# Kernel optimization log

Measured on AMD Instinct MI355X. Metric: run time of the kernel, lower is better.

Reference implementation:

```python
import jax, jax.numpy as jnp
import numpy as np

DIM = 512
BATCH, SEQ = 4, 4096


def setup_inputs() -> dict:
    key = jax.random.key(0)
    kx, kq, kk, kv, ko = jax.random.split(key, 5)
    s = DIM ** -0.5  # fan-in style init scale for stability
    return {
        "x": jax.random.normal(kx, (BATCH, SEQ, DIM), dtype=jnp.float32),
        "Wq": jax.random.normal(kq, (DIM, DIM), dtype=jnp.float32) * s,
        "Wk": jax.random.normal(kk, (DIM, DIM), dtype=jnp.float32) * s,
        "Wv": jax.random.normal(kv, (DIM, DIM), dtype=jnp.float32) * s,
        "Wo": jax.random.normal(ko, (DIM, DIM), dtype=jnp.float32) * s,
    }


def reference(x, Wq, Wk, Wv, Wo):
    # x: [B, S, D]; projections (torch Linear, no bias -> x @ W here)
    q = jnp.einsum('bsd,dk->bsk', x, Wq)  # [B,S,K]
    k = jnp.einsum('bsd,dk->bsk', x, Wk)  # [B,S,K]
    v = jnp.einsum('bsd,dv->bsv', x, Wv)  # [B,S,V]

    # sequential recurrence: M_t = M_{t-1} + v_t k_t^T ; y_t = M_t q_t
    def step(M, qkv_t):
        q_t, k_t, v_t = qkv_t  # each [B, K] / [B, V]
        M = M + v_t[:, :, None] * k_t[:, None, :]  # [B, V, K]
        y_t = jnp.einsum('bvk,bk->bv', M, q_t)
        return M, y_t

    M0 = jnp.zeros((x.shape[0], Wv.shape[1], Wk.shape[1]), dtype=x.dtype)
    qT = jnp.swapaxes(q, 0, 1)  # [S,B,K]
    kT = jnp.swapaxes(k, 0, 1)
    vT = jnp.swapaxes(v, 0, 1)
    _, ys = jax.lax.scan(step, M0, (qT, kT, vT))  # ys: [S,B,V]
    y = jnp.swapaxes(ys, 0, 1)  # [B,S,V]
    return jnp.einsum('bsv,vd->bsd', y, Wo)
```

## Files before the change

### kernel.cpp

```cpp
#include <hip/hip_runtime.h>
#include <hip/hip_bf16.h>

typedef __attribute__((ext_vector_type(8))) short bf16x8;
typedef __attribute__((ext_vector_type(4))) float f32x4;

__device__ inline short f2bf(float f) {
    __hip_bfloat16 h = __float2bfloat16(f);
    short s;
    __builtin_memcpy(&s, &h, 2);
    return s;
}
__device__ inline float bf2f(short s) {
    unsigned int u = ((unsigned int)(unsigned short)s) << 16;
    float f;
    __builtin_memcpy(&f, &u, 4);
    return f;
}

__device__ inline void cp16_async(const void* g, void* l) {
    __builtin_amdgcn_global_load_lds(
        (const __attribute__((address_space(1))) void*)g,
        (__attribute__((address_space(3))) void*)l, 16, 0, 0);
}


__global__ void cast_x_kernel(const float* __restrict__ x, short* __restrict__ out, int n4) {
    int i = blockIdx.x * 256 + threadIdx.x;
    if (i < n4) {
        float4 f = ((const float4*)x)[i];
        union { short s[4]; int2 v; } u;
        u.s[0] = f2bf(f.x); u.s[1] = f2bf(f.y); u.s[2] = f2bf(f.z); u.s[3] = f2bf(f.w);
        ((int2*)out)[i] = u.v;
    }
}

__global__ void transpose_cast_w4(const float* __restrict__ W0, const float* __restrict__ W1,
                                  const float* __restrict__ W2, const float* __restrict__ W3,
                                  short* __restrict__ W4T) {
    int i = blockIdx.x * 256 + threadIdx.x;
    int w = i >> 18;
    int r = i & 262143;
    int n = r >> 9, k = r & 511;
    const float* W = (w == 0) ? W0 : (w == 1) ? W1 : (w == 2) ? W2 : W3;
    W4T[i] = f2bf(W[k * 512 + n]);
}

__global__ void transpose_bf16(const short* __restrict__ in, short* __restrict__ out) {
    __shared__ short sT[64][72];
    const int t0 = blockIdx.x * 64, f0 = blockIdx.y * 64, b = blockIdx.z;
    const short* ip = in + (size_t)b * 4096 * 512;
    short* op = out + (size_t)b * 512 * 4096;
#pragma unroll
    for (int p = 0; p < 2; ++p) {
        int lin = p * 256 + threadIdx.x;
        int row = lin >> 3, col8 = (lin & 7) * 8;
        short tmp[8];
        *(int4*)tmp = *(const int4*)&ip[(size_t)(t0 + row) * 512 + f0 + col8];
#pragma unroll
        for (int s = 0; s < 8; ++s) sT[col8 + s][row] = tmp[s];
    }
    __syncthreads();
#pragma unroll
    for (int p = 0; p < 2; ++p) {
        int lin = p * 256 + threadIdx.x;
        int fr = lin >> 3, tc8 = (lin & 7) * 8;
        int4 v = *(const int4*)&sT[fr][tc8];
        *(int4*)&op[(size_t)(f0 + fr) * 4096 + t0 + tc8] = v;
    }
}


#define LDS_DECL __shared__ short sA0[4096], sA1[4096], sB0[4096], sB1[4096]

__device__ inline void mfma_kloop64(const short* __restrict__ A, int lda,
                                    const short* __restrict__ B, int ldb,
                                    int Kd, f32x4* acc,
                                    short* sA0, short* sA1, short* sB0, short* sB1) {
    const int tid = threadIdx.x, lane = tid & 63, wv = tid >> 6;
    const int quad = lane >> 4, lr = lane & 15;
    const int wr = (wv >> 1) * 64, wc = (wv & 1) * 64;
    const int c0 = tid, c1 = tid + 256;
    const int r0 = c0 >> 2, k80 = (c0 & 3) * 8;
    const int r1 = c1 >> 2, k81 = (c1 & 3) * 8;

    for (int k0 = 0; k0 < Kd; k0 += 64) {
        __syncthreads();
        cp16_async(A + (size_t)r0 * lda + k0 + k80,      sA0 + c0 * 8);
        cp16_async(A + (size_t)r1 * lda + k0 + k81,      sA0 + c1 * 8);
        cp16_async(A + (size_t)r0 * lda + k0 + 32 + k80, sA1 + c0 * 8);
        cp16_async(A + (size_t)r1 * lda + k0 + 32 + k81, sA1 + c1 * 8);
        cp16_async(B + (size_t)r0 * ldb + k0 + k80,      sB0 + c0 * 8);
        cp16_async(B + (size_t)r1 * ldb + k0 + k81,      sB0 + c1 * 8);
        cp16_async(B + (size_t)r0 * ldb + k0 + 32 + k80, sB1 + c0 * 8);
        cp16_async(B + (size_t)r1 * ldb + k0 + 32 + k81, sB1 + c1 * 8);
        __syncthreads();
#pragma unroll
        for (int half = 0; half < 2; ++half) {
            const short* pa = half ? sA1 : sA0;
            const short* pb = half ? sB1 : sB0;
            bf16x8 af[4], bfr[4];
#pragma unroll
            for (int i = 0; i < 4; ++i)
                af[i] = *(const bf16x8*)&pa[(wr + i * 16 + lr) * 32 + quad * 8];
#pragma unroll
            for (int j = 0; j < 4; ++j)
                bfr[j] = *(const bf16x8*)&pb[(wc + j * 16 + lr) * 32 + quad * 8];
#pragma unroll
            for (int i = 0; i < 4; ++i)
#pragma unroll
                for (int j = 0; j < 4; ++j)
                    acc[i * 4 + j] = __builtin_amdgcn_mfma_f32_16x16x32_bf16(af[i], bfr[j], acc[i * 4 + j], 0, 0, 0);
        }
    }
}

__device__ inline void store_out(float* p, float v) { *p = v; }
__device__ inline void store_out(short* p, float v) { *p = f2bf(v); }

template <typename OutT>
__device__ inline void store_tile128(OutT* C, int ldc, const f32x4* acc) {
    const int lane = threadIdx.x & 63, wv = threadIdx.x >> 6;
    const int quad = lane >> 4, lr = lane & 15;
    const int wr = (wv >> 1) * 64, wc = (wv & 1) * 64;
#pragma unroll
    for (int i = 0; i < 4; ++i)
#pragma unroll
        for (int j = 0; j < 4; ++j)
#pragma unroll
            for (int r = 0; r < 4; ++r)
                store_out(&C[(size_t)(wr + i * 16 + quad * 4 + r) * ldc + wc + j * 16 + lr],
                          acc[i * 4 + j][r]);
}


__global__ __launch_bounds__(256, 2) void gemm_qk(const short* __restrict__ Xb,
                                                  const short* __restrict__ WqkT,
                                                  short* __restrict__ Qb, short* __restrict__ Kb) {
    LDS_DECL;
    const short* At = Xb + (size_t)blockIdx.x * 128 * 512;
    const short* Bt = WqkT + (size_t)blockIdx.y * 128 * 512;
    short* Cbase = (blockIdx.y < 4) ? Qb : Kb;
    int n0 = (blockIdx.y & 3) * 128;
    short* Ct = Cbase + (size_t)blockIdx.x * 128 * 512 + n0;
    f32x4 acc[16];
#pragma unroll
    for (int i = 0; i < 16; ++i) acc[i] = (f32x4){0.f, 0.f, 0.f, 0.f};
    mfma_kloop64(At, 512, Bt, 512, 512, acc, sA0, sA1, sB0, sB1);
    store_tile128(Ct, 512, acc);
}

__global__ __launch_bounds__(256, 2) void gemm_vt(const short* __restrict__ WvT,
                                                  const short* __restrict__ Xb,
                                                  short* __restrict__ Vt) {
    LDS_DECL;
    const int b = blockIdx.z;
    const short* At = WvT + (size_t)blockIdx.x * 128 * 512;
    const short* Bt = Xb + ((size_t)b * 4096 + blockIdx.y * 128) * 512;
    short* Ct = Vt + (size_t)b * 512 * 4096 + (size_t)blockIdx.x * 128 * 4096 + blockIdx.y * 128;
    f32x4 acc[16];
#pragma unroll
    for (int i = 0; i < 16; ++i) acc[i] = (f32x4){0.f, 0.f, 0.f, 0.f};
    mfma_kloop64(At, 512, Bt, 512, 512, acc, sA0, sA1, sB0, sB1);
    store_tile128(Ct, 4096, acc);
}

template <typename OutT>
__global__ __launch_bounds__(256, 2) void gemm128(const short* __restrict__ A, int lda,
                                                  const short* __restrict__ B, int ldb,
                                                  OutT* __restrict__ C, int ldc, int Kd) {
    LDS_DECL;
    const short* At = A + (size_t)blockIdx.x * 128 * lda;
    const short* Bt = B + (size_t)blockIdx.y * 128 * ldb;
    OutT* Ct = C + (size_t)blockIdx.x * 128 * ldc + blockIdx.y * 128;
    f32x4 acc[16];
#pragma unroll
    for (int i = 0; i < 16; ++i) acc[i] = (f32x4){0.f, 0.f, 0.f, 0.f};
    mfma_kloop64(At, lda, Bt, ldb, Kd, acc, sA0, sA1, sB0, sB1);
    store_tile128(Ct, ldc, acc);
}


__global__ __launch_bounds__(256, 2) void phaseA(const short* __restrict__ Vt,
                                                 const short* __restrict__ Kt,
                                                 short* __restrict__ AM) {
    LDS_DECL;
    const int bc = blockIdx.z, b = bc >> 4, c = bc & 15;
    const short* Ap = Vt + ((size_t)b * 512 + blockIdx.x * 128) * 4096 + c * 256;
    const short* Bp = Kt + ((size_t)b * 512 + blockIdx.y * 128) * 4096 + c * 256;
    short* Cp = AM + (size_t)bc * 262144 + (size_t)blockIdx.x * 128 * 512 + blockIdx.y * 128;
    f32x4 acc[16];
#pragma unroll
    for (int i = 0; i < 16; ++i) acc[i] = (f32x4){0.f, 0.f, 0.f, 0.f};
    mfma_kloop64(Ap, 4096, Bp, 4096, 256, acc, sA0, sA1, sB0, sB1);
    store_tile128(Cp, 512, acc);
}

__global__ void scan_kernel(short* __restrict__ AM) {
    int i = blockIdx.x * 256 + threadIdx.x;
    int b = i >> 15;
    int vk8 = i & 32767;
    size_t base = (size_t)b * 16 * 262144 + (size_t)vk8 * 8;
    float acc[8];
#pragma unroll
    for (int s = 0; s < 8; ++s) acc[s] = 0.f;
    for (int c = 0; c < 16; ++c) {
        short* p = AM + base + (size_t)c * 262144;
        short in8[8];
        *(int4*)in8 = *(const int4*)p;
        short out8[8];
#pragma unroll
        for (int s = 0; s < 8; ++s) out8[s] = f2bf(acc[s]);
        *(int4*)p = *(const int4*)out8;
#pragma unroll
        for (int s = 0; s < 8; ++s) acc[s] += bf2f(in8[s]);
    }
}

__global__ __launch_bounds__(256, 2) void phaseS(const short* __restrict__ Q,
                                                 const short* __restrict__ K,
                                                 short* __restrict__ P) {
    LDS_DECL;
    const int bc = blockIdx.z, b = bc >> 4, c = bc & 15;
    const int mt = blockIdx.x, nt = blockIdx.y;
    if (mt < nt) return;
    short* Pt = P + (size_t)bc * 65536 + (size_t)mt * 128 * 256 + nt * 128;
    const short* Ap = Q + ((size_t)(b * 4096 + c * 256 + mt * 128)) * 512;
    const short* Bp = K + ((size_t)(b * 4096 + c * 256 + nt * 128)) * 512;
    f32x4 acc[16];
#pragma unroll
    for (int i = 0; i < 16; ++i) acc[i] = (f32x4){0.f, 0.f, 0.f, 0.f};
    mfma_kloop64(Ap, 512, Bp, 512, 512, acc, sA0, sA1, sB0, sB1);
    const int lane = threadIdx.x & 63, wv = threadIdx.x >> 6;
    const int quad = lane >> 4, lr = lane & 15;
    const int wr = (wv >> 1) * 64, wc = (wv & 1) * 64;
    const bool diag = (mt == nt);
#pragma unroll
    for (int i = 0; i < 4; ++i)
#pragma unroll
        for (int j = 0; j < 4; ++j)
#pragma unroll
            for (int r = 0; r < 4; ++r) {
                int t = wr + i * 16 + quad * 4 + r;
                int jj = wc + j * 16 + lr;
                float v = (!diag || jj <= t) ? acc[i * 4 + j][r] : 0.f;
                Pt[(size_t)t * 256 + jj] = f2bf(v);
            }
}

__global__ __launch_bounds__(256, 2) void phaseY(const short* __restrict__ Q,
                                                 const short* __restrict__ Mpre,
                                                 const short* __restrict__ P,
                                                 const short* __restrict__ Vt,
                                                 short* __restrict__ Y) {
    LDS_DECL;
    const int bc = blockIdx.z, b = bc >> 4, c = bc & 15;
    const int mt = blockIdx.x, nt = blockIdx.y;
    f32x4 acc[16];
#pragma unroll
    for (int i = 0; i < 16; ++i) acc[i] = (f32x4){0.f, 0.f, 0.f, 0.f};
    const short* Ai = Q + ((size_t)(b * 4096 + c * 256 + mt * 128)) * 512;
    const short* Bi = Mpre + (size_t)bc * 262144 + (size_t)nt * 128 * 512;
    mfma_kloop64(Ai, 512, Bi, 512, 512, acc, sA0, sA1, sB0, sB1);
    const short* Ap = P + (size_t)bc * 65536 + (size_t)mt * 128 * 256;
    const short* Bv = Vt + ((size_t)b * 512 + nt * 128) * 4096 + c * 256;
    mfma_kloop64(Ap, 256, Bv, 4096, (mt + 1) * 128, acc, sA0, sA1, sB0, sB1);
    short* Cp = Y + ((size_t)(b * 4096 + c * 256 + mt * 128)) * 512 + nt * 128;
    store_tile128(Cp, 512, acc);
}


extern "C" void kernel_launch(void* const* d_in, const int* in_sizes, int n_in,
                              void* d_out, int out_size, void* d_ws, size_t ws_size,
                              hipStream_t stream) {
    const float* x  = (const float*)d_in[0];
    const float* Wq = (const float*)d_in[1];
    const float* Wk = (const float*)d_in[2];
    const float* Wv = (const float*)d_in[3];
    const float* Wo = (const float*)d_in[4];
    float* out = (float*)d_out;

    const size_t NTD = 16384 * 512;

    short* ws  = (short*)d_ws;
    short* Xb  = ws;
    short* Qb  = Xb + NTD;
    short* Kb  = Qb + NTD;
    short* Kt  = Kb + NTD;
    short* Vt  = Kt + NTD;
    short* P   = Vt + NTD;
    short* W4T = P + 4194304;
    short* AM  = W4T + 1048576;
    short* Yb  = Kb;

    short* WqT = W4T;
    short* WvT = W4T + 2 * 262144;
    short* WoT = W4T + 3 * 262144;

    cast_x_kernel<<<8192, 256, 0, stream>>>(x, Xb, (int)(NTD / 4));
    transpose_cast_w4<<<4096, 256, 0, stream>>>(Wq, Wk, Wv, Wo, W4T);

    gemm_qk<<<dim3(128, 8), 256, 0, stream>>>(Xb, WqT, Qb, Kb);
    gemm_vt<<<dim3(4, 32, 4), 256, 0, stream>>>(WvT, Xb, Vt);
    transpose_bf16<<<dim3(64, 8, 4), 256, 0, stream>>>(Kb, Kt);

    phaseA<<<dim3(4, 4, 64), 256, 0, stream>>>(Vt, Kt, AM);
    scan_kernel<<<512, 256, 0, stream>>>(AM);
    phaseS<<<dim3(2, 2, 64), 256, 0, stream>>>(Qb, Kb, P);
    phaseY<<<dim3(2, 4, 64), 256, 0, stream>>>(Qb, AM, P, Vt, Yb);

    gemm128<float><<<dim3(128, 4), 256, 0, stream>>>(Yb, 512, WoT, 512, out, 512, 512);
}
```

Before: 231.5 us.

## Merge independent launches and compute K transpose via extra GEMM instead of transpose kernel

Merges the x cast and weight transpose-cast into one prep kernel, and merges the Q/K, V^T projections into one launch that also computes K^T directly as Wk^T·X^T. This replaces the separate transpose_bf16 pass. It also co-schedules the chunk-state prefix scan with the intra-chunk QK^T score kernel in one grid, since they are independent. The goal is fewer launches and more concurrency. The cost is an extra 512-block GEMM for K^T instead of a cheap memory transpose, plus uneven block types within each grid.

Measured after the change: 222.2 us. -4.0%, faster.

```diff
diff --git a/kernel.cpp b/kernel.cpp
--- a/kernel.cpp
+++ b/kernel.cpp
@@ -24,48 +24,24 @@
 }
 
 
-__global__ void cast_x_kernel(const float* __restrict__ x, short* __restrict__ out, int n4) {
-    int i = blockIdx.x * 256 + threadIdx.x;
-    if (i < n4) {
+__global__ void prep_kernel(const float* __restrict__ x, short* __restrict__ Xb,
+                            const float* __restrict__ W0, const float* __restrict__ W1,
+                            const float* __restrict__ W2, const float* __restrict__ W3,
+                            short* __restrict__ W4T) {
+    int bid = blockIdx.x;
+    if (bid < 8192) {
+        int i = bid * 256 + threadIdx.x;
         float4 f = ((const float4*)x)[i];
         union { short s[4]; int2 v; } u;
         u.s[0] = f2bf(f.x); u.s[1] = f2bf(f.y); u.s[2] = f2bf(f.z); u.s[3] = f2bf(f.w);
-        ((int2*)out)[i] = u.v;
-    }
-}
-
-__global__ void transpose_cast_w4(const float* __restrict__ W0, const float* __restrict__ W1,
-                                  const float* __restrict__ W2, const float* __restrict__ W3,
-                                  short* __restrict__ W4T) {
-    int i = blockIdx.x * 256 + threadIdx.x;
-    int w = i >> 18;
-    int r = i & 262143;
-    int n = r >> 9, k = r & 511;
-    const float* W = (w == 0) ? W0 : (w == 1) ? W1 : (w == 2) ? W2 : W3;
-    W4T[i] = f2bf(W[k * 512 + n]);
-}
-
-__global__ void transpose_bf16(const short* __restrict__ in, short* __restrict__ out) {
-    __shared__ short sT[64][72];
-    const int t0 = blockIdx.x * 64, f0 = blockIdx.y * 64, b = blockIdx.z;
-    const short* ip = in + (size_t)b * 4096 * 512;
-    short* op = out + (size_t)b * 512 * 4096;
-#pragma unroll
-    for (int p = 0; p < 2; ++p) {
-        int lin = p * 256 + threadIdx.x;
-        int row = lin >> 3, col8 = (lin & 7) * 8;
-        short tmp[8];
-        *(int4*)tmp = *(const int4*)&ip[(size_t)(t0 + row) * 512 + f0 + col8];
-#pragma unroll
-        for (int s = 0; s < 8; ++s) sT[col8 + s][row] = tmp[s];
-    }
-    __syncthreads();
-#pragma unroll
-    for (int p = 0; p < 2; ++p) {
-        int lin = p * 256 + threadIdx.x;
-        int fr = lin >> 3, tc8 = (lin & 7) * 8;
-        int4 v = *(const int4*)&sT[fr][tc8];
-        *(int4*)&op[(size_t)(f0 + fr) * 4096 + t0 + tc8] = v;
+        ((int2*)Xb)[i] = u.v;
+    } else {
+        int i = (bid - 8192) * 256 + threadIdx.x;
+        int w = i >> 18;
+        int r = i & 262143;
+        int n = r >> 9, k = r & 511;
+        const float* W = (w == 0) ? W0 : (w == 1) ? W1 : (w == 2) ? W2 : W3;
+        W4T[i] = f2bf(W[k * 512 + n]);
     }
 }
 
@@ -132,51 +108,33 @@
                           acc[i * 4 + j][r]);
 }
 
-
-__global__ __launch_bounds__(256, 2) void gemm_qk(const short* __restrict__ Xb,
-                                                  const short* __restrict__ WqkT,
-                                                  short* __restrict__ Qb, short* __restrict__ Kb) {
-    LDS_DECL;
-    const short* At = Xb + (size_t)blockIdx.x * 128 * 512;
-    const short* Bt = WqkT + (size_t)blockIdx.y * 128 * 512;
-    short* Cbase = (blockIdx.y < 4) ? Qb : Kb;
-    int n0 = (blockIdx.y & 3) * 128;
-    short* Ct = Cbase + (size_t)blockIdx.x * 128 * 512 + n0;
-    f32x4 acc[16];
-#pragma unroll
-    for (int i = 0; i < 16; ++i) acc[i] = (f32x4){0.f, 0.f, 0.f, 0.f};
-    mfma_kloop64(At, 512, Bt, 512, 512, acc, sA0, sA1, sB0, sB1);
-    store_tile128(Ct, 512, acc);
-}
-
-__global__ __launch_bounds__(256, 2) void gemm_vt(const short* __restrict__ WvT,
-                                                  const short* __restrict__ Xb,
-                                                  short* __restrict__ Vt) {
-    LDS_DECL;
-    const int b = blockIdx.z;
-    const short* At = WvT + (size_t)blockIdx.x * 128 * 512;
-    const short* Bt = Xb + ((size_t)b * 4096 + blockIdx.y * 128) * 512;
-    short* Ct = Vt + (size_t)b * 512 * 4096 + (size_t)blockIdx.x * 128 * 4096 + blockIdx.y * 128;
-    f32x4 acc[16];
-#pragma unroll
-    for (int i = 0; i < 16; ++i) acc[i] = (f32x4){0.f, 0.f, 0.f, 0.f};
-    mfma_kloop64(At, 512, Bt, 512, 512, acc, sA0, sA1, sB0, sB1);
-    store_tile128(Ct, 4096, acc);
-}
-
-template <typename OutT>
-__global__ __launch_bounds__(256, 2) void gemm128(const short* __restrict__ A, int lda,
-                                                  const short* __restrict__ B, int ldb,
-                                                  OutT* __restrict__ C, int ldc, int Kd) {
-    LDS_DECL;
-    const short* At = A + (size_t)blockIdx.x * 128 * lda;
-    const short* Bt = B + (size_t)blockIdx.y * 128 * ldb;
-    OutT* Ct = C + (size_t)blockIdx.x * 128 * ldc + blockIdx.y * 128;
-    f32x4 acc[16];
-#pragma unroll
-    for (int i = 0; i < 16; ++i) acc[i] = (f32x4){0.f, 0.f, 0.f, 0.f};
-    mfma_kloop64(At, lda, Bt, ldb, Kd, acc, sA0, sA1, sB0, sB1);
-    store_tile128(Ct, ldc, acc);
+__global__ __launch_bounds__(256, 2) void proj_all(const short* __restrict__ Xb,
+                                                   const short* __restrict__ W4T,
+                                                   short* __restrict__ Qb, short* __restrict__ Kb,
+                                                   short* __restrict__ Vt, short* __restrict__ Kt) {
+    LDS_DECL;
+    f32x4 acc[16];
+#pragma unroll
+    for (int i = 0; i < 16; ++i) acc[i] = (f32x4){0.f, 0.f, 0.f, 0.f};
+    const int bid = blockIdx.x;
+    if (bid < 1024) {
+        const int mt = bid >> 3, by = bid & 7;
+        const short* At = Xb + (size_t)mt * 128 * 512;
+        const short* Bt = W4T + (size_t)by * 128 * 512;
+        short* Ct = ((by < 4) ? Qb : Kb) + (size_t)mt * 128 * 512 + (by & 3) * 128;
+        mfma_kloop64(At, 512, Bt, 512, 512, acc, sA0, sA1, sB0, sB1);
+        store_tile128(Ct, 512, acc);
+    } else {
+        const int g = bid - 1024;
+        const int which = g >> 9;
+        const int r = g & 511;
+        const int b = r & 3, tt = (r >> 2) & 31, ft = r >> 7;
+        const short* At = W4T + (size_t)(which ? 1 : 2) * 262144 + (size_t)ft * 128 * 512;
+        const short* Bt = Xb + ((size_t)b * 4096 + tt * 128) * 512;
+        short* Ct = (which ? Kt : Vt) + (size_t)b * 512 * 4096 + (size_t)ft * 128 * 4096 + tt * 128;
+        mfma_kloop64(At, 512, Bt, 512, 512, acc, sA0, sA1, sB0, sB1);
+        store_tile128(Ct, 4096, acc);
+    }
 }
 
 
@@ -195,34 +153,36 @@
     store_tile128(Cp, 512, acc);
 }
 
-__global__ void scan_kernel(short* __restrict__ AM) {
-    int i = blockIdx.x * 256 + threadIdx.x;
-    int b = i >> 15;
-    int vk8 = i & 32767;
-    size_t base = (size_t)b * 16 * 262144 + (size_t)vk8 * 8;
-    float acc[8];
-#pragma unroll
-    for (int s = 0; s < 8; ++s) acc[s] = 0.f;
-    for (int c = 0; c < 16; ++c) {
-        short* p = AM + base + (size_t)c * 262144;
-        short in8[8];
-        *(int4*)in8 = *(const int4*)p;
-        short out8[8];
-#pragma unroll
-        for (int s = 0; s < 8; ++s) out8[s] = f2bf(acc[s]);
-        *(int4*)p = *(const int4*)out8;
-#pragma unroll
-        for (int s = 0; s < 8; ++s) acc[s] += bf2f(in8[s]);
-    }
-}
-
-__global__ __launch_bounds__(256, 2) void phaseS(const short* __restrict__ Q,
-                                                 const short* __restrict__ K,
-                                                 short* __restrict__ P) {
-    LDS_DECL;
-    const int bc = blockIdx.z, b = bc >> 4, c = bc & 15;
-    const int mt = blockIdx.x, nt = blockIdx.y;
+__global__ __launch_bounds__(256, 2) void scan_phaseS(short* __restrict__ AM,
+                                                      const short* __restrict__ Q,
+                                                      const short* __restrict__ K,
+                                                      short* __restrict__ P) {
+    LDS_DECL;
+    if (blockIdx.x < 512) {
+        int i = blockIdx.x * 256 + threadIdx.x;
+        int b = i >> 15;
+        int vk8 = i & 32767;
+        size_t base = (size_t)b * 16 * 262144 + (size_t)vk8 * 8;
+        float acc[8];
+#pragma unroll
+        for (int s = 0; s < 8; ++s) acc[s] = 0.f;
+        for (int c = 0; c < 16; ++c) {
+            short* p = AM + base + (size_t)c * 262144;
+            short in8[8];
+            *(int4*)in8 = *(const int4*)p;
+            short out8[8];
+#pragma unroll
+            for (int s = 0; s < 8; ++s) out8[s] = f2bf(acc[s]);
+            *(int4*)p = *(const int4*)out8;
+#pragma unroll
+            for (int s = 0; s < 8; ++s) acc[s] += bf2f(in8[s]);
+        }
+        return;
+    }
+    const int e = blockIdx.x - 512;
+    const int bc = e >> 2, mt = e & 1, nt = (e >> 1) & 1;
     if (mt < nt) return;
+    const int b = bc >> 4, c = bc & 15;
     short* Pt = P + (size_t)bc * 65536 + (size_t)mt * 128 * 256 + nt * 128;
     const short* Ap = Q + ((size_t)(b * 4096 + c * 256 + mt * 128)) * 512;
     const short* Bp = K + ((size_t)(b * 4096 + c * 256 + nt * 128)) * 512;
@@ -266,6 +226,21 @@
     mfma_kloop64(Ap, 256, Bv, 4096, (mt + 1) * 128, acc, sA0, sA1, sB0, sB1);
     short* Cp = Y + ((size_t)(b * 4096 + c * 256 + mt * 128)) * 512 + nt * 128;
     store_tile128(Cp, 512, acc);
+}
+
+template <typename OutT>
+__global__ __launch_bounds__(256, 2) void gemm128(const short* __restrict__ A, int lda,
+                                                  const short* __restrict__ B, int ldb,
+                                                  OutT* __restrict__ C, int ldc, int Kd) {
+    LDS_DECL;
+    const short* At = A + (size_t)blockIdx.x * 128 * lda;
+    const short* Bt = B + (size_t)blockIdx.y * 128 * ldb;
+    OutT* Ct = C + (size_t)blockIdx.x * 128 * ldc + blockIdx.y * 128;
+    f32x4 acc[16];
+#pragma unroll
+    for (int i = 0; i < 16; ++i) acc[i] = (f32x4){0.f, 0.f, 0.f, 0.f};
+    mfma_kloop64(At, lda, Bt, ldb, Kd, acc, sA0, sA1, sB0, sB1);
+    store_tile128(Ct, ldc, acc);
 }
 
 
@@ -292,21 +267,12 @@
     short* AM  = W4T + 1048576;
     short* Yb  = Kb;
 
-    short* WqT = W4T;
-    short* WvT = W4T + 2 * 262144;
     short* WoT = W4T + 3 * 262144;
 
-    cast_x_kernel<<<8192, 256, 0, stream>>>(x, Xb, (int)(NTD / 4));
-    transpose_cast_w4<<<4096, 256, 0, stream>>>(Wq, Wk, Wv, Wo, W4T);
-
-    gemm_qk<<<dim3(128, 8), 256, 0, stream>>>(Xb, WqT, Qb, Kb);
-    gemm_vt<<<dim3(4, 32, 4), 256, 0, stream>>>(WvT, Xb, Vt);
-    transpose_bf16<<<dim3(64, 8, 4), 256, 0, stream>>>(Kb, Kt);
-
+    prep_kernel<<<12288, 256, 0, stream>>>(x, Xb, Wq, Wk, Wv, Wo, W4T);
+    proj_all<<<2048, 256, 0, stream>>>(Xb, W4T, Qb, Kb, Vt, Kt);
     phaseA<<<dim3(4, 4, 64), 256, 0, stream>>>(Vt, Kt, AM);
-    scan_kernel<<<512, 256, 0, stream>>>(AM);
-    phaseS<<<dim3(2, 2, 64), 256, 0, stream>>>(Qb, Kb, P);
+    scan_phaseS<<<768, 256, 0, stream>>>(AM, Qb, Kb, P);
     phaseY<<<dim3(2, 4, 64), 256, 0, stream>>>(Qb, AM, P, Vt, Yb);
-
     gemm128<float><<<dim3(128, 4), 256, 0, stream>>>(Yb, 512, WoT, 512, out, 512, 512);
 }
```
